# Kernel tuning notes

Hardware: AMD Instinct MI355X
Metric: run time of the kernel (lower is better)

The kernel has to match this reference:

```python
import jax, jax.numpy as jnp
import numpy as np

WH = 7; WW = 7; N = WH * WW          # window tokens
C = 256; H = 8; D = C // H            # dim, heads, head_dim
SCALE = D ** -0.5
B = 4096                              # batch * num_windows
EPS = 1e-12


def _relative_position_index():
    coords = np.stack(np.meshgrid(np.arange(WH), np.arange(WW), indexing='ij'))  # [2,WH,WW]
    cf = coords.reshape(2, -1)                                                   # [2,N]
    rc = (cf[:, :, None] - cf[:, None, :]).transpose(1, 2, 0).astype(np.int64)   # [N,N,2]
    rc[..., 0] += WH - 1
    rc[..., 1] += WW - 1
    rc[..., 0] *= 2 * WW - 1
    return jnp.asarray(rc.sum(-1), jnp.int32)                                    # [N,N]


def _l2n_heads(x):
    # F.normalize default dim=1: normalize over the HEADS axis of [B,H,N,D]
    n = jnp.sqrt(jnp.sum(x * x, axis=1, keepdims=True))
    return x / jnp.maximum(n, EPS)


def setup_inputs() -> dict:
    key = jax.random.key(0)
    ks = jax.random.split(key, 12)
    p = lambda k, s: (0.02 * jax.random.normal(k, s, dtype=jnp.float32))
    return {
        'x1': jax.random.normal(ks[0], (B, N, C), dtype=jnp.float32),
        'x2': jax.random.normal(ks[1], (B, N, C), dtype=jnp.float32),
        'rel_index': _relative_position_index(),
        'kv1_w': p(ks[2], (2 * C, C)), 'kv1_b': jnp.zeros((2 * C,), jnp.float32),
        'kv2_w': p(ks[3], (2 * C, C)), 'kv2_b': jnp.zeros((2 * C,), jnp.float32),
        'q_w': p(ks[4], (C, C)), 'q_b': jnp.zeros((C,), jnp.float32),
        'rpb_table': p(ks[5], ((2 * WH - 1) * (2 * WW - 1), H)),
        'proj1_w': p(ks[6], (C, C)), 'proj1_b': jnp.zeros((C,), jnp.float32),
        'proj2_w': p(ks[7], (C, C)), 'proj2_b': jnp.zeros((C,), jnp.float32),
    }


def reference(x1, x2, rel_index, kv1_w, kv1_b, kv2_w, kv2_b, q_w, q_b,
              rpb_table, proj1_w, proj1_b, proj1=None, proj2=None, **_unused):
    del proj1, proj2
    raise NotImplementedError


def _forward(x1, x2, rel_index, kv1_w, kv1_b, kv2_w, kv2_b, q_w, q_b,
             rpb_table, proj1_w, proj1_b, proj2_w, proj2_b):
    def split_kv(x, w, b):
        kv = (x @ w.T + b).reshape(B, N, 2, H, D).transpose(2, 0, 3, 1, 4)  # [2,B,H,N,D]
        return kv[0], kv[1]

    k1, v1 = split_kv(x1, kv1_w, kv1_b)
    k2, v2 = split_kv(x2, kv2_w, kv2_b)

    q = (jnp.abs(x2 - x1) @ q_w.T + q_b).reshape(B, N, H, D).transpose(0, 2, 1, 3)  # [B,H,N,D]
    q = q * SCALE

    bias = rpb_table[rel_index.reshape(-1)].reshape(N, N, H).transpose(2, 0, 1)  # [H,N,N]

    # branch 1: attend q -> k2/v2
    attn = jnp.einsum('bhnd,bhmd->bhnm', _l2n_heads(q), _l2n_heads(k2)) + bias[None]
    attn = jax.nn.softmax(attn, axis=-1)
    o1 = (jnp.einsum('bhnm,bhmd->bhnd', attn, v2) - q).transpose(0, 2, 1, 3).reshape(B, N, C)
    o1 = o1 @ proj1_w.T + proj1_b

    # branch 2: q rescaled again, attend -> k1/v1
    q = q * SCALE
    attn = jnp.einsum('bhnd,bhmd->bhnm', _l2n_heads(q), _l2n_heads(k1)) + bias[None]
    attn = jax.nn.softmax(attn, axis=-1)
    o2 = (jnp.einsum('bhnm,bhmd->bhnd', attn, v1) - q).transpose(0, 2, 1, 3).reshape(B, N, C)
    o2 = o2 @ proj2_w.T + proj2_b
    return o1, o2


def reference(x1, x2, rel_index, kv1_w, kv1_b, kv2_w, kv2_b, q_w, q_b,
              rpb_table, proj1_w, proj1_b, proj2_w, proj2_b):
    return _forward(x1, x2, rel_index, kv1_w, kv1_b, kv2_w, kv2_b, q_w, q_b,
                    rpb_table, proj1_w, proj1_b, proj2_w, proj2_b)
```

## Files before the change

kernel.cpp:

```cpp
#include <hip/hip_runtime.h>
#include <hip/hip_bf16.h>


typedef __attribute__((ext_vector_type(8))) short short8;
typedef __attribute__((ext_vector_type(4))) float f32x4;

#define NTOK 49
#define NWIN 4096
#define MROWS 200704
#define NMT 3136
#define SCALE 0.17677669529663687f

#define TQ_T   0
#define TKV1_T 16
#define TKV2_T 48
#define TP1_T  80
#define TP2_T  96

#define OFF_BIAS_B 917504ull
#define OFF_QN_B   1048576ull
#define OFF_NRM_B  103809024ull
#define OFF_KN2_B  129499136ull
#define OFF_KN1_B  232259584ull
#define OFF_V2_B   335020032ull
#define OFF_V1_B   437780480ull

__device__ __forceinline__ short f2b(float f) {
    union { float f; unsigned u; } v{f};
    unsigned r = v.u + 0x7fffu + ((v.u >> 16) & 1u);
    return (short)(r >> 16);
}
__device__ __forceinline__ float b2f(short s) {
    return __uint_as_float(((unsigned)(unsigned short)s) << 16);
}
__device__ __forceinline__ short8 pack8(float4 a, float4 b) {
    short8 s;
    s[0]=f2b(a.x); s[1]=f2b(a.y); s[2]=f2b(a.z); s[3]=f2b(a.w);
    s[4]=f2b(b.x); s[5]=f2b(b.y); s[6]=f2b(b.z); s[7]=f2b(b.w);
    return s;
}
__device__ __forceinline__ f32x4 mfma16(short8 a, short8 b, f32x4 c) {
    return __builtin_amdgcn_mfma_f32_16x16x32_bf16(a, b, c, 0, 0, 0);
}
__device__ __forceinline__ short8 g16(const short* p) { return *(const short8*)p; }
__device__ __forceinline__ short8 ld16r128(const short* base, int row, int m8) {
    return *(const short8*)((const char*)base + row*128 + ((m8*2) ^ ((row&7)<<4)));
}
__device__ __forceinline__ void st2r128(short* base, int row, int m, short v) {
    *(short*)((char*)base + row*128 + ((m*2) ^ ((row&7)<<4))) = v;
}
__device__ __forceinline__ void gl16(const void* g, void* l) {
    __builtin_amdgcn_global_load_lds(
        (const __attribute__((address_space(1))) unsigned*)g,
        (__attribute__((address_space(3))) unsigned*)l, 16, 0, 0);
}
__device__ __forceinline__ short8 ldb(const short* tile, int lr, int lg, int kb) {
    return *(const short8*)((const char*)tile + lr*512
                            + ((kb*64 + lg*16) ^ ((lr&7)<<4)));
}

__global__ void prep_w(const float* __restrict__ qw, const float* __restrict__ kv1,
                       const float* __restrict__ kv2, const float* __restrict__ p1,
                       const float* __restrict__ p2, short* __restrict__ ws) {
    int i = blockIdx.x * 256 + threadIdx.x;
    int e = i * 8;
    const float* src; int rel, tbase;
    if      (e < 65536)  { src = qw;  rel = e;          tbase = TQ_T;  }
    else if (e < 196608) { src = kv1; rel = e - 65536;  tbase = TKV1_T; }
    else if (e < 327680) { src = kv2; rel = e - 196608; tbase = TKV2_T; }
    else if (e < 393216) { src = p1;  rel = e - 327680; tbase = TP1_T; }
    else                 { src = p2;  rel = e - 393216; tbase = TP2_T; }
    int row = rel >> 8, col = rel & 255;
    short8 v;
#pragma unroll
    for (int k = 0; k < 8; ++k) v[k] = f2b(src[rel + k]);
    char* dst = (char*)ws + (size_t)(tbase + (row >> 4)) * 8192
              + (row & 15) * 512 + ((col * 2) ^ ((row & 7) << 4));
    *(short8*)dst = v;
}

__global__ void k_bias(const int* __restrict__ rel_index,
                       const float* __restrict__ rpb, short* __restrict__ ws) {
    int i = blockIdx.x * 256 + threadIdx.x;
    int r  = i & 3;
    int nt = (i >> 2) & 3;
    int lr = (i >> 4) & 15;
    int lg = (i >> 8) & 3;
    int mt = (i >> 10) & 3;
    int h  = (i >> 12) & 7;
    int m  = 16*mt + 4*lg + r;
    int mc = 16*nt + lr;
    float v = 0.f;
    if (m < NTOK && mc < NTOK) v = rpb[rel_index[m*NTOK + mc]*8 + h];
    ((float*)((char*)ws + OFF_BIAS_B))[i] = v;
}

__global__ __launch_bounds__(256, 2)
void k_qkv(const float* __restrict__ x1, const float* __restrict__ x2,
           const float* __restrict__ kv1_b, const float* __restrict__ kv2_b,
           const float* __restrict__ q_b, short* __restrict__ ws)
{
    __shared__ short Bt[2][4096];

    const int t    = (int)threadIdx.x;
    const int wv   = t >> 6;
    const int lane = t & 63;
    const int lr   = t & 15;
    const int lg   = (t >> 4) & 3;
    const int bid  = (int)blockIdx.x;
    const int type = bid % 3;
    const int mt   = bid / 3;
    const int ar   = mt*64 + 16*wv + lr;

    unsigned widr[4], tokr[4];
#pragma unroll
    for (int r = 0; r < 4; ++r) {
        unsigned n = (unsigned)(mt*64 + 16*wv + 4*lg + r);
        widr[r] = n / 49u; tokr[r] = n - widr[r]*49u;
    }

    const char* tb = (const char*)ws
        + (size_t)(type == 0 ? TQ_T : (type == 1 ? TKV2_T : TKV1_T)) * 8192;

#define STAGE(J, B) do {                                                  \
        const char* g_ = tb + (size_t)(J)*8192 + wv*2048 + lane*16;       \
        char* l_ = (char*)Bt[(B)] + wv*2048 + lane*16;                    \
        gl16(g_, l_); gl16(g_ + 1024, l_ + 1024);                         \
    } while (0)

    if (type == 0) {
        short8 ad[8];
#pragma unroll
        for (int kb = 0; kb < 8; ++kb) {
            const float* pa = x2 + (size_t)ar*256 + kb*32 + lg*8;
            const float* pc = x1 + (size_t)ar*256 + kb*32 + lg*8;
            float4 a0 = *(const float4*)pa, a1 = *(const float4*)(pa+4);
            float4 c0 = *(const float4*)pc, c1 = *(const float4*)(pc+4);
            float4 d0 = make_float4(fabsf(a0.x-c0.x), fabsf(a0.y-c0.y),
                                    fabsf(a0.z-c0.z), fabsf(a0.w-c0.w));
            float4 d1 = make_float4(fabsf(a1.x-c1.x), fabsf(a1.y-c1.y),
                                    fabsf(a1.z-c1.z), fabsf(a1.w-c1.w));
            ad[kb] = pack8(d0, d1);
        }
        STAGE(0, 0);
        __syncthreads();
        f32x4 qa[16];
#pragma unroll
        for (int j = 0; j < 16; ++j) {
            if (j < 15) STAGE(j+1, (j+1)&1);
            const short* bt = Bt[j&1];
            f32x4 acc = {0.f,0.f,0.f,0.f};
#pragma unroll
            for (int kb = 0; kb < 8; ++kb) acc = mfma16(ad[kb], ldb(bt, lr, lg, kb), acc);
            float bj = q_b[j*16 + lr];
#pragma unroll
            for (int r = 0; r < 4; ++r) acc[r] = (acc[r] + bj) * SCALE;
            qa[j] = acc;
            __syncthreads();
        }
        short* qn  = (short*)((char*)ws + OFF_QN_B);
        float* nrm = (float*)((char*)ws + OFF_NRM_B);
#pragma unroll
        for (int r = 0; r < 4; ++r) {
            float s0 = 0.f, s1 = 0.f;
#pragma unroll
            for (int jj = 0; jj < 8; ++jj) {
                float v0 = qa[2*jj][r], v1 = qa[2*jj+1][r];
                s0 = fmaf(v0, v0, s0); s1 = fmaf(v1, v1, s1);
            }
            float n0 = fmaxf(sqrtf(s0), 1e-12f), n1 = fmaxf(sqrtf(s1), 1e-12f);
            unsigned n = widr[r]*49u + tokr[r];
            nrm[(size_t)n*32 + lr]      = n0;
            nrm[(size_t)n*32 + 16 + lr] = n1;
            float ri0 = 1.0f/n0, ri1 = 1.0f/n1;
            size_t base = ((size_t)widr[r]*392 + tokr[r])*32;
#pragma unroll
            for (int j = 0; j < 16; ++j) {
                int h = j >> 1, p = j & 1;
                qn[base + h*1568 + 16*p + lr] = f2b(qa[j][r] * (p ? ri1 : ri0));
            }
        }
    } else {
        const float* xp  = (type == 1) ? x2 : x1;
        const float* kvb = (type == 1) ? kv2_b : kv1_b;
        short* knp = (short*)((char*)ws + ((type == 1) ? OFF_KN2_B : OFF_KN1_B));
        short* vp  = (short*)((char*)ws + ((type == 1) ? OFF_V2_B  : OFF_V1_B));

        short8 ad[8];
#pragma unroll
        for (int kb = 0; kb < 8; ++kb) {
            const float* pa = xp + (size_t)ar*256 + kb*32 + lg*8;
            float4 a0 = *(const float4*)pa, a1 = *(const float4*)(pa+4);
            ad[kb] = pack8(a0, a1);
        }
        size_t base[4];
#pragma unroll
        for (int r = 0; r < 4; ++r) base[r] = ((size_t)widr[r]*392 + tokr[r])*32;

        STAGE(0, 0);
        __syncthreads();
        f32x4 ka[16];
#pragma unroll
        for (int j = 0; j < 32; ++j) {
            if (j < 31) STAGE(j+1, (j+1)&1);
            const short* bt = Bt[j&1];
            f32x4 acc = {0.f,0.f,0.f,0.f};
#pragma unroll
            for (int kb = 0; kb < 8; ++kb) acc = mfma16(ad[kb], ldb(bt, lr, lg, kb), acc);
            if (j < 16) {
                float bj = kvb[j*16 + lr];
#pragma unroll
                for (int r = 0; r < 4; ++r) acc[r] += bj;
                ka[j] = acc;
            } else {
                const int jv = j - 16;
                float bj = kvb[256 + jv*16 + lr];
                int h = jv >> 1, p = jv & 1;
#pragma unroll
                for (int r = 0; r < 4; ++r)
                    vp[base[r] + h*1568 + 16*p + lr] = f2b(acc[r] + bj);
            }
            __syncthreads();
        }
#pragma unroll
        for (int r = 0; r < 4; ++r) {
            float s0 = 0.f, s1 = 0.f;
#pragma unroll
            for (int jj = 0; jj < 8; ++jj) {
                float v0 = ka[2*jj][r], v1 = ka[2*jj+1][r];
                s0 = fmaf(v0, v0, s0); s1 = fmaf(v1, v1, s1);
            }
            float ri0 = 1.0f/fmaxf(sqrtf(s0), 1e-12f);
            float ri1 = 1.0f/fmaxf(sqrtf(s1), 1e-12f);
#pragma unroll
            for (int j = 0; j < 16; ++j) {
                int h = j >> 1, p = j & 1;
                knp[base[r] + h*1568 + 16*p + lr] = f2b(ka[j][r] * (p ? ri1 : ri0));
            }
        }
    }
#undef STAGE
}

__global__ __launch_bounds__(512, 2)
void k_attn(short* __restrict__ ws)
{
    __shared__ short OP[NTOK*256];
    __shared__ short PS[8*16*64];

    const int t  = (int)threadIdx.x;
    const int h  = t >> 6;
    const int lr = t & 15;
    const int lg = (t >> 4) & 3;
    const int bid = (int)blockIdx.x;
    const int wid = bid >> 1;
    const int br  = bid & 1;

    const short* qn  = (const short*)((const char*)ws + OFF_QN_B);
    const float* nrm = (const float*)((const char*)ws + OFF_NRM_B);
    const float* bias_t = (const float*)((const char*)ws + OFF_BIAS_B);
    short* Pb = PS + h*1024;
    const int khbase = (wid*8 + h)*49;

    const short* knp = (const short*)((const char*)ws + (br ? OFF_KN1_B : OFF_KN2_B));
    const short* vp  = (const short*)((const char*)ws + (br ? OFF_V1_B  : OFF_V2_B));
    short* opre = (short*)((char*)ws + (br ? OFF_KN1_B : OFF_KN2_B));
    const float subscale = br ? SCALE : 1.0f;

    short8 kf[4];
#pragma unroll
    for (int nt = 0; nt < 4; ++nt) {
        int n = min(16*nt + lr, NTOK-1);
        kf[nt] = g16(knp + (size_t)(khbase + n)*32 + lg*8);
    }
    short8 vf[2][2];
#pragma unroll
    for (int dt = 0; dt < 2; ++dt)
#pragma unroll
        for (int st = 0; st < 2; ++st) {
            short8 s8;
#pragma unroll
            for (int e = 0; e < 8; ++e) {
                int tok = st*32 + lg*8 + e;
                short v_ = 0;
                if (tok < NTOK) v_ = vp[(size_t)(khbase + tok)*32 + 16*dt + lr];
                s8[e] = v_;
            }
            vf[dt][st] = s8;
        }

#pragma unroll 1
    for (int mt = 0; mt < 4; ++mt) {
        int mrow = min(16*mt + lr, NTOK-1);
        short8 aq = g16(qn + (size_t)(khbase + mrow)*32 + lg*8);
        f32x4 S[4];
#pragma unroll
        for (int nt = 0; nt < 4; ++nt) {
            f32x4 z = {0.f,0.f,0.f,0.f};
            S[nt] = mfma16(aq, kf[nt], z);
        }
        const float4* bp4 = (const float4*)(bias_t + ((((h*4 + mt)*4 + lg)*16) + lr)*16);
        float4 bv[4];
#pragma unroll
        for (int nt = 0; nt < 4; ++nt) bv[nt] = bp4[nt];
        float sv[4][4];
#pragma unroll
        for (int nt = 0; nt < 4; ++nt) {
            bool ms = (16*nt + lr) >= NTOK;
            sv[nt][0] = ms ? -1e30f : (S[nt][0] + bv[nt].x);
            sv[nt][1] = ms ? -1e30f : (S[nt][1] + bv[nt].y);
            sv[nt][2] = ms ? -1e30f : (S[nt][2] + bv[nt].z);
            sv[nt][3] = ms ? -1e30f : (S[nt][3] + bv[nt].w);
        }
        float isum[4];
#pragma unroll
        for (int r = 0; r < 4; ++r) {
            float mx = fmaxf(fmaxf(sv[0][r], sv[1][r]), fmaxf(sv[2][r], sv[3][r]));
#pragma unroll
            for (int d = 1; d < 16; d <<= 1) mx = fmaxf(mx, __shfl_xor(mx, d));
            float e0 = __expf(sv[0][r]-mx), e1 = __expf(sv[1][r]-mx);
            float e2 = __expf(sv[2][r]-mx), e3 = __expf(sv[3][r]-mx);
            float sm = (e0+e1) + (e2+e3);
#pragma unroll
            for (int d = 1; d < 16; d <<= 1) sm += __shfl_xor(sm, d);
            isum[r] = 1.0f / sm;
            int pr = 4*lg + r;
            st2r128(Pb, pr,      lr, f2b(e0));
            st2r128(Pb, pr, 16 + lr, f2b(e1));
            st2r128(Pb, pr, 32 + lr, f2b(e2));
            st2r128(Pb, pr, 48 + lr, f2b(e3));
        }
        short8 pa0 = ld16r128(Pb, lr, lg*8);
        short8 pa1 = ld16r128(Pb, lr, 32 + lg*8);
#pragma unroll
        for (int dt = 0; dt < 2; ++dt) {
            f32x4 acc = {0.f,0.f,0.f,0.f};
            acc = mfma16(pa0, vf[dt][0], acc);
            acc = mfma16(pa1, vf[dt][1], acc);
#pragma unroll
            for (int r = 0; r < 4; ++r) {
                int m = 16*mt + 4*lg + r;
                int me = min(m, NTOK-1);
                int d = 16*dt + lr;
                float qv = b2f(qn[(size_t)(khbase + me)*32 + d]);
                float nv = nrm[((size_t)wid*NTOK + me)*32 + d];
                float o = acc[r]*isum[r] - qv*nv*subscale;
                if (m < NTOK) OP[m*256 + h*32 + d] = f2b(o);
            }
        }
    }
    __syncthreads();
    {
        const short8* sp = (const short8*)OP;
        short8* dp = (short8*)(opre + (size_t)wid*NTOK*256);
        for (int i = t; i < NTOK*256/8; i += 512) dp[i] = sp[i];
    }
}

__global__ __launch_bounds__(256, 2)
void k_proj(const float* __restrict__ p1_b, const float* __restrict__ p2_b,
            const short* __restrict__ ws, float* __restrict__ out)
{
    __shared__ short Bt[2][4096];

    const int t    = (int)threadIdx.x;
    const int wv   = t >> 6;
    const int lane = t & 63;
    const int lr   = t & 15;
    const int lg   = (t >> 4) & 3;
    const int bid  = (int)blockIdx.x;
    const int br   = bid & 1;
    const int mt   = bid >> 1;
    const int ar   = mt*64 + 16*wv + lr;

    const char* tb = (const char*)ws + (size_t)(br ? TP2_T : TP1_T) * 8192;
    const short* op  = (const short*)((const char*)ws + (br ? OFF_KN1_B : OFF_KN2_B));
    const float* pjb = br ? p2_b : p1_b;
    float* outp = out + (size_t)br*((size_t)MROWS*256);

    short8 ad[8];
#pragma unroll
    for (int kb = 0; kb < 8; ++kb) ad[kb] = g16(op + (size_t)ar*256 + kb*32 + lg*8);

#define STAGE(J, B) do {                                                  \
        const char* g_ = tb + (size_t)(J)*8192 + wv*2048 + lane*16;       \
        char* l_ = (char*)Bt[(B)] + wv*2048 + lane*16;                    \
        gl16(g_, l_); gl16(g_ + 1024, l_ + 1024);                         \
    } while (0)

    STAGE(0, 0);
    __syncthreads();
#pragma unroll 1
    for (int j = 0; j < 16; ++j) {
        if (j < 15) STAGE(j+1, (j+1)&1);
        const short* bt = Bt[j&1];
        f32x4 acc = {0.f,0.f,0.f,0.f};
#pragma unroll
        for (int kb = 0; kb < 8; ++kb) acc = mfma16(ad[kb], ldb(bt, lr, lg, kb), acc);
        float bj = pjb[j*16 + lr];
#pragma unroll
        for (int r = 0; r < 4; ++r) {
            int n = mt*64 + 16*wv + 4*lg + r;
            outp[(size_t)n*256 + j*16 + lr] = acc[r] + bj;
        }
        __syncthreads();
    }
#undef STAGE
}

extern "C" void kernel_launch(void* const* d_in, const int* in_sizes, int n_in,
                              void* d_out, int out_size, void* d_ws, size_t ws_size,
                              hipStream_t stream) {
    (void)in_sizes; (void)n_in; (void)ws_size; (void)out_size;
    const float* x1   = (const float*)d_in[0];
    const float* x2   = (const float*)d_in[1];
    const int*   rel  = (const int*)  d_in[2];
    const float* kv1w = (const float*)d_in[3];
    const float* kv1b = (const float*)d_in[4];
    const float* kv2w = (const float*)d_in[5];
    const float* kv2b = (const float*)d_in[6];
    const float* qw   = (const float*)d_in[7];
    const float* qb   = (const float*)d_in[8];
    const float* rpb  = (const float*)d_in[9];
    const float* p1w  = (const float*)d_in[10];
    const float* p1b  = (const float*)d_in[11];
    const float* p2w  = (const float*)d_in[12];
    const float* p2b  = (const float*)d_in[13];
    float* out = (float*)d_out;
    short* ws  = (short*)d_ws;

    hipLaunchKernelGGL(prep_w, dim3(224), dim3(256), 0, stream,
                       qw, kv1w, kv2w, p1w, p2w, ws);
    hipLaunchKernelGGL(k_bias, dim3(128), dim3(256), 0, stream,
                       rel, rpb, ws);
    hipLaunchKernelGGL(k_qkv, dim3(NMT*3), dim3(256), 0, stream,
                       x1, x2, kv1b, kv2b, qb, ws);
    hipLaunchKernelGGL(k_attn, dim3(NWIN*2), dim3(512), 0, stream, ws);
    hipLaunchKernelGGL(k_proj, dim3(NMT*2), dim3(256), 0, stream,
                       p1b, p2b, (const short*)ws, out);
}
```

Measured before the change: 900.2 us.

## Fuse Q, KV1 and KV2 projections into one block per row tile

```diff
diff --git a/kernel.cpp b/kernel.cpp
--- a/kernel.cpp
+++ b/kernel.cpp
@@ -107,47 +107,52 @@
     const int lane = t & 63;
     const int lr   = t & 15;
     const int lg   = (t >> 4) & 3;
-    const int bid  = (int)blockIdx.x;
-    const int type = bid % 3;
-    const int mt   = bid / 3;
+    const int mt   = (int)blockIdx.x;
     const int ar   = mt*64 + 16*wv + lr;
 
     unsigned widr[4], tokr[4];
+    size_t base[4];
 #pragma unroll
     for (int r = 0; r < 4; ++r) {
         unsigned n = (unsigned)(mt*64 + 16*wv + 4*lg + r);
         widr[r] = n / 49u; tokr[r] = n - widr[r]*49u;
-    }
-
-    const char* tb = (const char*)ws
-        + (size_t)(type == 0 ? TQ_T : (type == 1 ? TKV2_T : TKV1_T)) * 8192;
-
-#define STAGE(J, B) do {                                                  \
-        const char* g_ = tb + (size_t)(J)*8192 + wv*2048 + lane*16;       \
+        base[r] = ((size_t)widr[r]*392 + tokr[r])*32;
+    }
+
+#define STAGE(TB, J, B) do {                                              \
+        const char* g_ = (TB) + (size_t)(J)*8192 + wv*2048 + lane*16;     \
         char* l_ = (char*)Bt[(B)] + wv*2048 + lane*16;                    \
         gl16(g_, l_); gl16(g_ + 1024, l_ + 1024);                         \
     } while (0)
 
-    if (type == 0) {
+    short8 x2f[8], x1f[8];
+#pragma unroll
+    for (int kb = 0; kb < 8; ++kb) {
+        const float* pa = x2 + (size_t)ar*256 + kb*32 + lg*8;
+        const float* pc = x1 + (size_t)ar*256 + kb*32 + lg*8;
+        float4 a0 = *(const float4*)pa, a1 = *(const float4*)(pa+4);
+        float4 c0 = *(const float4*)pc, c1 = *(const float4*)(pc+4);
+        x2f[kb] = pack8(a0, a1);
+        x1f[kb] = pack8(c0, c1);
+    }
+
+    {
         short8 ad[8];
 #pragma unroll
         for (int kb = 0; kb < 8; ++kb) {
-            const float* pa = x2 + (size_t)ar*256 + kb*32 + lg*8;
-            const float* pc = x1 + (size_t)ar*256 + kb*32 + lg*8;
-            float4 a0 = *(const float4*)pa, a1 = *(const float4*)(pa+4);
-            float4 c0 = *(const float4*)pc, c1 = *(const float4*)(pc+4);
-            float4 d0 = make_float4(fabsf(a0.x-c0.x), fabsf(a0.y-c0.y),
-                                    fabsf(a0.z-c0.z), fabsf(a0.w-c0.w));
-            float4 d1 = make_float4(fabsf(a1.x-c1.x), fabsf(a1.y-c1.y),
-                                    fabsf(a1.z-c1.z), fabsf(a1.w-c1.w));
-            ad[kb] = pack8(d0, d1);
-        }
-        STAGE(0, 0);
+            short8 d;
+#pragma unroll
+            for (int e = 0; e < 8; ++e)
+                d[e] = f2b(fabsf(b2f(x2f[kb][e]) - b2f(x1f[kb][e])));
+            ad[kb] = d;
+        }
+        const char* tb = (const char*)ws + (size_t)TQ_T * 8192;
+        STAGE(tb, 0, 0);
         __syncthreads();
         f32x4 qa[16];
 #pragma unroll
         for (int j = 0; j < 16; ++j) {
-            if (j < 15) STAGE(j+1, (j+1)&1);
+            if (j < 15) STAGE(tb, j+1, (j+1)&1);
             const short* bt = Bt[j&1];
             f32x4 acc = {0.f,0.f,0.f,0.f};
 #pragma unroll
@@ -173,40 +178,32 @@
             nrm[(size_t)n*32 + lr]      = n0;
             nrm[(size_t)n*32 + 16 + lr] = n1;
             float ri0 = 1.0f/n0, ri1 = 1.0f/n1;
-            size_t base = ((size_t)widr[r]*392 + tokr[r])*32;
 #pragma unroll
             for (int j = 0; j < 16; ++j) {
                 int h = j >> 1, p = j & 1;
-                qn[base + h*1568 + 16*p + lr] = f2b(qa[j][r] * (p ? ri1 : ri0));
-            }
-        }
-    } else {
-        const float* xp  = (type == 1) ? x2 : x1;
-        const float* kvb = (type == 1) ? kv2_b : kv1_b;
-        short* knp = (short*)((char*)ws + ((type == 1) ? OFF_KN2_B : OFF_KN1_B));
-        short* vp  = (short*)((char*)ws + ((type == 1) ? OFF_V2_B  : OFF_V1_B));
-
-        short8 ad[8];
-#pragma unroll
-        for (int kb = 0; kb < 8; ++kb) {
-            const float* pa = xp + (size_t)ar*256 + kb*32 + lg*8;
-            float4 a0 = *(const float4*)pa, a1 = *(const float4*)(pa+4);
-            ad[kb] = pack8(a0, a1);
-        }
-        size_t base[4];
-#pragma unroll
-        for (int r = 0; r < 4; ++r) base[r] = ((size_t)widr[r]*392 + tokr[r])*32;
-
-        STAGE(0, 0);
+                qn[base[r] + h*1568 + 16*p + lr] = f2b(qa[j][r] * (p ? ri1 : ri0));
+            }
+        }
+    }
+
+#pragma unroll 1
+    for (int src = 0; src < 2; ++src) {
+        const float* kvb = src ? kv1_b : kv2_b;
+        const char* tb = (const char*)ws + (size_t)(src ? TKV1_T : TKV2_T) * 8192;
+        short* knp = (short*)((char*)ws + (src ? OFF_KN1_B : OFF_KN2_B));
+        short* vp  = (short*)((char*)ws + (src ? OFF_V1_B  : OFF_V2_B));
+        const short8* adp = src ? x1f : x2f;
+
+        STAGE(tb, 0, 0);
         __syncthreads();
         f32x4 ka[16];
 #pragma unroll
         for (int j = 0; j < 32; ++j) {
-            if (j < 31) STAGE(j+1, (j+1)&1);
+            if (j < 31) STAGE(tb, j+1, (j+1)&1);
             const short* bt = Bt[j&1];
             f32x4 acc = {0.f,0.f,0.f,0.f};
 #pragma unroll
-            for (int kb = 0; kb < 8; ++kb) acc = mfma16(ad[kb], ldb(bt, lr, lg, kb), acc);
+            for (int kb = 0; kb < 8; ++kb) acc = mfma16(adp[kb], ldb(bt, lr, lg, kb), acc);
             if (j < 16) {
                 float bj = kvb[j*16 + lr];
 #pragma unroll
@@ -433,7 +430,7 @@
                        qw, kv1w, kv2w, p1w, p2w, ws);
     hipLaunchKernelGGL(k_bias, dim3(128), dim3(256), 0, stream,
                        rel, rpb, ws);
-    hipLaunchKernelGGL(k_qkv, dim3(NMT*3), dim3(256), 0, stream,
+    hipLaunchKernelGGL(k_qkv, dim3(NMT), dim3(256), 0, stream,
                        x1, x2, kv1b, kv2b, qb, ws);
     hipLaunchKernelGGL(k_attn, dim3(NWIN*2), dim3(512), 0, stream, ws);
     hipLaunchKernelGGL(k_proj, dim3(NMT*2), dim3(256), 0, stream,
```

New measurement: 1.220 ms. 35.6% more time.
